# Optimization experiments

Measured on AMD Instinct MI355X. Metric: run time of the kernel, lower is better.

The kernel has to match this reference:

```python
import jax, jax.numpy as jnp
import numpy as np


def setup_inputs() -> dict:
    key = jax.random.key(0)
    kx, kw, kb = jax.random.split(key, 3)
    x = jax.random.normal(kx, (32, 256, 64, 64), dtype=jnp.float32)
    # Conv2d(in=2, out=1, kernel=7) weights, OIHW layout
    W = jax.random.normal(kw, (1, 2, 7, 7), dtype=jnp.float32) * 0.1
    b = jax.random.normal(kb, (1,), dtype=jnp.float32) * 0.1
    return {"x": x, "W": W, "b": b}


def reference(x, W, b):
    # Channel-wise max and mean pooling -> [B, 1, H, W] each
    maxpool = jnp.max(x, axis=1, keepdims=True)
    avgpool = jnp.mean(x, axis=1, keepdims=True)
    pool = jnp.concatenate([maxpool, avgpool], axis=1)  # [B, 2, H, W]
    # 7x7 conv, stride 1, padding 3 (SAME), NCHW / OIHW
    samap = jax.lax.conv_general_dilated(
        pool, W,
        window_strides=(1, 1),
        padding=[(3, 3), (3, 3)],
        dimension_numbers=("NCHW", "OIHW", "NCHW"),
    ) + b[None, :, None, None]
    samap = jax.nn.sigmoid(samap)  # [B, 1, H, W]
    return x * samap
```

## Files before the change

### kernel.cpp

```cpp
#include <hip/hip_runtime.h>
#include <math.h>

constexpr int B_  = 32;
constexpr int C_  = 256;
constexpr int H_  = 64;
constexpr int W_  = 64;
constexpr int HW_ = H_ * W_;
constexpr size_t CHW_ = (size_t)C_ * HW_;

typedef float v4f __attribute__((ext_vector_type(4)));

__global__ __launch_bounds__(512) void pool_kernel(const float* __restrict__ x,
                                                   float* __restrict__ pool) {
    const int blk  = blockIdx.x;
    const int b    = blk >> 4;
    const int h0   = (blk & 15) * 4;
    const int tid  = threadIdx.x;
    const int wv   = tid >> 6;
    const int lane = tid & 63;

    const float* base = x + (size_t)b * CHW_ + (size_t)(wv * 32) * HW_ + h0 * W_ + lane * 4;
    float4 v  = *(const float4*)base;
    float4 mx = v, sm = v;
#pragma unroll
    for (int c = 1; c < 32; ++c) {
        float4 u = *(const float4*)(base + (size_t)c * HW_);
        mx.x = fmaxf(mx.x, u.x); mx.y = fmaxf(mx.y, u.y);
        mx.z = fmaxf(mx.z, u.z); mx.w = fmaxf(mx.w, u.w);
        sm.x += u.x; sm.y += u.y; sm.z += u.z; sm.w += u.w;
    }

    __shared__ float4 lmax[8][64];
    __shared__ float4 lsum[8][64];
    lmax[wv][lane] = mx;
    lsum[wv][lane] = sm;
    __syncthreads();

    if (tid < 64) {
        float4 M = lmax[0][tid], S = lsum[0][tid];
#pragma unroll
        for (int g = 1; g < 8; ++g) {
            float4 m2 = lmax[g][tid], s2 = lsum[g][tid];
            M.x = fmaxf(M.x, m2.x); M.y = fmaxf(M.y, m2.y);
            M.z = fmaxf(M.z, m2.z); M.w = fmaxf(M.w, m2.w);
            S.x += s2.x; S.y += s2.y; S.z += s2.z; S.w += s2.w;
        }
        const float inv = 1.0f / 256.0f;
        float4 A = make_float4(S.x * inv, S.y * inv, S.z * inv, S.w * inv);
        const int r   = tid >> 4;
        const int col = (tid & 15) * 4;
        float* pm = pool + (size_t)b * 2 * HW_ + (h0 + r) * W_ + col;
        *(float4*)pm         = M;
        *(float4*)(pm + HW_) = A;
    }
}

__global__ __launch_bounds__(512) void conv_scale_kernel(const float* __restrict__ x,
                                                         const float* __restrict__ pool,
                                                         const float* __restrict__ Wp,
                                                         const float* __restrict__ bp,
                                                         float* __restrict__ out) {
    const int blk  = blockIdx.x;
    const int b    = blk >> 4;
    const int h0   = (blk & 15) * 4;
    const int tid  = threadIdx.x;
    const int wv   = tid >> 6;
    const int lane = tid & 63;

    __shared__ float sw[98];
    __shared__ float spool[2][10][64];
    __shared__ float ssa[256];

    if (tid < 98) sw[tid] = Wp[tid];
    for (int idx = tid; idx < 1280; idx += 512) {
        const int plane = idx / 640;
        const int rem   = idx - plane * 640;
        const int r     = rem >> 6;
        const int w     = rem & 63;
        const int hh    = h0 + r - 3;
        spool[plane][r][w] = (hh >= 0 && hh < H_)
            ? pool[((size_t)b * 2 + plane) * HW_ + hh * W_ + w] : 0.0f;
    }
    __syncthreads();

    if (tid < 256) {
        const int r   = tid >> 6;
        const int col = tid & 63;
        float acc = bp[0];
#pragma unroll
        for (int p = 0; p < 2; ++p) {
            const float* wc = sw + p * 49;
#pragma unroll
            for (int kh = 0; kh < 7; ++kh) {
                const float* prow = &spool[p][r + kh][0];
#pragma unroll
                for (int kw = 0; kw < 7; ++kw) {
                    const int ww = col + kw - 3;
                    if (ww >= 0 && ww < W_)
                        acc = fmaf(prow[ww], wc[kh * 7 + kw], acc);
                }
            }
        }
        ssa[tid] = 1.0f / (1.0f + expf(-acc));
    }
    __syncthreads();

    const float4 sv = ((const float4*)ssa)[lane];
    const size_t base = (size_t)b * CHW_ + (size_t)(wv * 32) * HW_ + h0 * W_ + lane * 4;
    const float* xb = x + base;
    float*       ob = out + base;
#pragma unroll
    for (int c = 0; c < 32; ++c) {
        const float4 xv = *(const float4*)(xb + (size_t)c * HW_);
        v4f ov;
        ov.x = xv.x * sv.x; ov.y = xv.y * sv.y;
        ov.z = xv.z * sv.z; ov.w = xv.w * sv.w;
        __builtin_nontemporal_store(ov, (v4f*)(ob + (size_t)c * HW_));
    }
}

extern "C" void kernel_launch(void* const* d_in, const int* in_sizes, int n_in,
                              void* d_out, int out_size, void* d_ws, size_t ws_size,
                              hipStream_t stream) {
    const float* x  = (const float*)d_in[0];
    const float* Wp = (const float*)d_in[1];
    const float* bp = (const float*)d_in[2];
    float* out = (float*)d_out;

    float* pool = (float*)d_ws;

    pool_kernel<<<B_ * (H_ / 4), 512, 0, stream>>>(x, pool);
    conv_scale_kernel<<<B_ * (H_ / 4), 512, 0, stream>>>(x, pool, Wp, bp, out);
}
```

Before: 257.5 us.

## Fuse pooling into conv-scale kernel with halo recompute and XCD-aware block remap

Merges the two kernels into one. Each block recomputes the channel max and mean for its 4 output rows plus a 3-row halo on each side (10 rows) straight from x, which drops the pool workspace round-trip and one launch. Each pooled row is reduced with wave shuffles across 4 channel groups of 64. Block indices are remapped so that consecutive hardware block IDs spread across the XCDs, aiming to keep neighbouring row tiles in a shared L2. The cost is about 2.5x redundant reads of x for the pooling phase, which may be served from cache, and the per-thread channel loop is longer and more serial.

```diff
diff --git a/kernel.cpp b/kernel.cpp
--- a/kernel.cpp
+++ b/kernel.cpp
@@ -10,57 +10,12 @@
 
 typedef float v4f __attribute__((ext_vector_type(4)));
 
-__global__ __launch_bounds__(512) void pool_kernel(const float* __restrict__ x,
-                                                   float* __restrict__ pool) {
-    const int blk  = blockIdx.x;
-    const int b    = blk >> 4;
-    const int h0   = (blk & 15) * 4;
-    const int tid  = threadIdx.x;
-    const int wv   = tid >> 6;
-    const int lane = tid & 63;
-
-    const float* base = x + (size_t)b * CHW_ + (size_t)(wv * 32) * HW_ + h0 * W_ + lane * 4;
-    float4 v  = *(const float4*)base;
-    float4 mx = v, sm = v;
-#pragma unroll
-    for (int c = 1; c < 32; ++c) {
-        float4 u = *(const float4*)(base + (size_t)c * HW_);
-        mx.x = fmaxf(mx.x, u.x); mx.y = fmaxf(mx.y, u.y);
-        mx.z = fmaxf(mx.z, u.z); mx.w = fmaxf(mx.w, u.w);
-        sm.x += u.x; sm.y += u.y; sm.z += u.z; sm.w += u.w;
-    }
-
-    __shared__ float4 lmax[8][64];
-    __shared__ float4 lsum[8][64];
-    lmax[wv][lane] = mx;
-    lsum[wv][lane] = sm;
-    __syncthreads();
-
-    if (tid < 64) {
-        float4 M = lmax[0][tid], S = lsum[0][tid];
-#pragma unroll
-        for (int g = 1; g < 8; ++g) {
-            float4 m2 = lmax[g][tid], s2 = lsum[g][tid];
-            M.x = fmaxf(M.x, m2.x); M.y = fmaxf(M.y, m2.y);
-            M.z = fmaxf(M.z, m2.z); M.w = fmaxf(M.w, m2.w);
-            S.x += s2.x; S.y += s2.y; S.z += s2.z; S.w += s2.w;
-        }
-        const float inv = 1.0f / 256.0f;
-        float4 A = make_float4(S.x * inv, S.y * inv, S.z * inv, S.w * inv);
-        const int r   = tid >> 4;
-        const int col = (tid & 15) * 4;
-        float* pm = pool + (size_t)b * 2 * HW_ + (h0 + r) * W_ + col;
-        *(float4*)pm         = M;
-        *(float4*)(pm + HW_) = A;
-    }
-}
-
-__global__ __launch_bounds__(512) void conv_scale_kernel(const float* __restrict__ x,
-                                                         const float* __restrict__ pool,
-                                                         const float* __restrict__ Wp,
-                                                         const float* __restrict__ bp,
-                                                         float* __restrict__ out) {
-    const int blk  = blockIdx.x;
+__global__ __launch_bounds__(512) void sam_fused(const float* __restrict__ x,
+                                                 const float* __restrict__ Wp,
+                                                 const float* __restrict__ bp,
+                                                 float* __restrict__ out) {
+    const int hwid = blockIdx.x;
+    const int blk  = (hwid & 7) * 64 + (hwid >> 3);
     const int b    = blk >> 4;
     const int h0   = (blk & 15) * 4;
     const int tid  = threadIdx.x;
@@ -68,18 +23,49 @@
     const int lane = tid & 63;
 
     __shared__ float sw[98];
-    __shared__ float spool[2][10][64];
-    __shared__ float ssa[256];
+    __shared__ __align__(16) float spool[2][10][64];
+    __shared__ __align__(16) float ssa[256];
 
     if (tid < 98) sw[tid] = Wp[tid];
-    for (int idx = tid; idx < 1280; idx += 512) {
-        const int plane = idx / 640;
-        const int rem   = idx - plane * 640;
-        const int r     = rem >> 6;
-        const int w     = rem & 63;
-        const int hh    = h0 + r - 3;
-        spool[plane][r][w] = (hh >= 0 && hh < H_)
-            ? pool[((size_t)b * 2 + plane) * HW_ + hh * W_ + w] : 0.0f;
+
+    const int g = lane & 15;
+    const int s = lane >> 4;
+    for (int r = wv; r < 10; r += 8) {
+        const int hh = h0 + r - 3;
+        if (hh >= 0 && hh < H_) {
+            const float* base = x + (size_t)b * CHW_ + (size_t)(s * 64) * HW_
+                                  + hh * W_ + g * 4;
+            float4 v  = *(const float4*)base;
+            float4 mx = v, sm = v;
+#pragma unroll 16
+            for (int c = 1; c < 64; ++c) {
+                float4 u = *(const float4*)(base + (size_t)c * HW_);
+                mx.x = fmaxf(mx.x, u.x); mx.y = fmaxf(mx.y, u.y);
+                mx.z = fmaxf(mx.z, u.z); mx.w = fmaxf(mx.w, u.w);
+                sm.x += u.x; sm.y += u.y; sm.z += u.z; sm.w += u.w;
+            }
+#pragma unroll
+            for (int m = 16; m <= 32; m <<= 1) {
+                mx.x = fmaxf(mx.x, __shfl_xor(mx.x, m));
+                mx.y = fmaxf(mx.y, __shfl_xor(mx.y, m));
+                mx.z = fmaxf(mx.z, __shfl_xor(mx.z, m));
+                mx.w = fmaxf(mx.w, __shfl_xor(mx.w, m));
+                sm.x += __shfl_xor(sm.x, m);
+                sm.y += __shfl_xor(sm.y, m);
+                sm.z += __shfl_xor(sm.z, m);
+                sm.w += __shfl_xor(sm.w, m);
+            }
+            if (s == 0) {
+                const float inv = 1.0f / 256.0f;
+                *(float4*)&spool[0][r][g * 4] = mx;
+                *(float4*)&spool[1][r][g * 4] =
+                    make_float4(sm.x * inv, sm.y * inv, sm.z * inv, sm.w * inv);
+            }
+        } else if (s == 0) {
+            const float4 z = make_float4(0.f, 0.f, 0.f, 0.f);
+            *(float4*)&spool[0][r][g * 4] = z;
+            *(float4*)&spool[1][r][g * 4] = z;
+        }
     }
     __syncthreads();
 
@@ -106,16 +92,15 @@
     __syncthreads();
 
     const float4 sv = ((const float4*)ssa)[lane];
-    const size_t base = (size_t)b * CHW_ + (size_t)(wv * 32) * HW_ + h0 * W_ + lane * 4;
-    const float* xb = x + base;
-    float*       ob = out + base;
-#pragma unroll
-    for (int c = 0; c < 32; ++c) {
-        const float4 xv = *(const float4*)(xb + (size_t)c * HW_);
+    const size_t rowbase = (size_t)b * CHW_ + (size_t)h0 * W_ + lane * 4;
+    for (int c = wv; c < C_; c += 8) {
+        const float* xb = x + rowbase + (size_t)c * HW_;
+        float*       ob = out + rowbase + (size_t)c * HW_;
+        const float4 xv = *(const float4*)xb;
         v4f ov;
         ov.x = xv.x * sv.x; ov.y = xv.y * sv.y;
         ov.z = xv.z * sv.z; ov.w = xv.w * sv.w;
-        __builtin_nontemporal_store(ov, (v4f*)(ob + (size_t)c * HW_));
+        __builtin_nontemporal_store(ov, (v4f*)ob);
     }
 }
 
@@ -126,9 +111,7 @@
     const float* Wp = (const float*)d_in[1];
     const float* bp = (const float*)d_in[2];
     float* out = (float*)d_out;
+    (void)d_ws; (void)ws_size;
 
-    float* pool = (float*)d_ws;
-
-    pool_kernel<<<B_ * (H_ / 4), 512, 0, stream>>>(x, pool);
-    conv_scale_kernel<<<B_ * (H_ / 4), 512, 0, stream>>>(x, pool, Wp, bp, out);
+    sam_fused<<<B_ * (H_ / 4), 512, 0, stream>>>(x, Wp, bp, out);
 }
```

New measurement: 254.7 us. Within noise of the previous version (-1.1%).
